# Performance work log

Hardware: AMD Instinct MI355X
Metric: run time of the kernel (lower is better)

## Reference

```python
import jax, jax.numpy as jnp
from jax import lax
import numpy as np

B, L, C = 16, 4096, 512
G = 8            # n_groups
CG = C // G      # group_dim = 64
WD = 4           # weather_dim
ORF = 10.0       # offset_range_factor


def conv1d(x, w, b=None):
    # x: [N, Cin, L], w: [Cout, Cin, 3], stride 1, padding 1
    y = lax.conv_general_dilated(x, w, window_strides=(1,), padding=[(1, 1)],
                                 dimension_numbers=('NCH', 'OIH', 'NCH'))
    if b is not None:
        y = y + b[None, :, None]
    return y


def group_norm(x, gamma, beta, groups=4, eps=1e-5):
    N, Cc, Ln = x.shape
    xr = x.reshape(N, groups, Cc // groups, Ln)
    mu = xr.mean(axis=(2, 3), keepdims=True)
    var = ((xr - mu) ** 2).mean(axis=(2, 3), keepdims=True)
    xn = ((xr - mu) / jnp.sqrt(var + eps)).reshape(N, Cc, Ln)
    return xn * gamma[None, :, None] + beta[None, :, None]


def grid_sample_bilinear_border(inp, grid):
    # Faithful torch F.grid_sample(mode='bilinear', padding_mode='border', align_corners=True)
    # inp: [N, C, H, W]; grid: [N, Ho, Wo, 2], grid[...,0]=x (width coord), grid[...,1]=y (height coord)
    N, Cc, H, W = inp.shape
    _, Ho, Wo, _ = grid.shape
    gx, gy = grid[..., 0], grid[..., 1]
    ix = jnp.clip((gx + 1.0) * 0.5 * (W - 1), 0.0, W - 1)  # border padding clamps coords
    iy = jnp.clip((gy + 1.0) * 0.5 * (H - 1), 0.0, H - 1)
    ix0f = jnp.floor(ix); iy0f = jnp.floor(iy)
    wx = ix - ix0f; wy = iy - iy0f
    ix0 = jnp.clip(ix0f.astype(jnp.int32), 0, W - 1)
    iy0 = jnp.clip(iy0f.astype(jnp.int32), 0, H - 1)
    ix1 = jnp.clip(ix0 + 1, 0, W - 1)
    iy1 = jnp.clip(iy0 + 1, 0, H - 1)
    flat = inp.reshape(N, Cc, H * W)
    def gather(iyk, ixk):
        idx = (iyk * W + ixk).reshape(N, 1, Ho * Wo)
        return jnp.take_along_axis(flat, idx, axis=2).reshape(N, Cc, Ho, Wo)
    v00 = gather(iy0, ix0); v01 = gather(iy0, ix1)
    v10 = gather(iy1, ix0); v11 = gather(iy1, ix1)
    wx = wx[:, None, :, :]; wy = wy[:, None, :, :]
    return (v00 * (1 - wy) * (1 - wx) + v01 * (1 - wy) * wx
            + v10 * wy * (1 - wx) + v11 * wy * wx)


def _forward(x, x_ext, w1, b1, gn_g, gn_b, w2, b2, w3, gate):
    xt = jnp.transpose(x, (0, 2, 1))              # [B, C, L]
    xg = xt.reshape(B * G, CG, L)                 # [B*G, CG, L]
    xe = jnp.transpose(x_ext, (0, 2, 1))          # [B, WD, L]
    xe = jnp.tile(xe, (G, 1, 1))                  # torch .repeat(n_groups,1,1)
    pin = jnp.concatenate([xg, xe], axis=1)       # [B*G, CG+WD, L]
    h = jax.nn.gelu(group_norm(conv1d(pin, w1, b1), gn_g, gn_b), approximate=False)
    h = jax.nn.gelu(conv1d(h, w2, b2), approximate=False)
    offset = jnp.tanh(conv1d(h, w3)) * ORF        # [B*G, 1, L]
    off_n = offset * (2.0 / (L - 1.0))
    ref = (jnp.linspace(0.5, L - 0.5, L, dtype=x.dtype) / (L - 1.0)) * 2.0 - 1.0
    grid_x = jnp.clip(ref[None, None, :, None] + off_n[..., None], -1.0, 1.0)  # [B*G,1,L,1]
    grid = jnp.concatenate([grid_x, jnp.zeros_like(grid_x)], axis=-1)
    grid = jnp.transpose(grid, (0, 2, 1, 3))      # [B*G, L, 1, 2]
    xs = grid_sample_bilinear_border(xg[..., None], grid)[..., 0]  # [B*G, CG, L]
    x_out = xg + jnp.tanh(gate) * xs
    x_out = x_out.reshape(B, C, L)
    return jnp.transpose(x_out, (0, 2, 1)), offset


def setup_inputs() -> dict:
    key = jax.random.key(0)
    ks = jax.random.split(key, 8)
    s = 0.05
    return {
        'x': jax.random.normal(ks[0], (B, L, C), jnp.float32),
        'x_ext': jax.random.normal(ks[1], (B, L, WD), jnp.float32),
        'w1': jax.random.normal(ks[2], (64, CG + WD, 3), jnp.float32) * s,
        'b1': jax.random.normal(ks[3], (64,), jnp.float32) * s,
        'gn_g': jnp.ones((64,), jnp.float32),
        'gn_b': jnp.zeros((64,), jnp.float32),
        'w2': jax.random.normal(ks[4], (32, 64, 3), jnp.float32) * s,
        'b2': jax.random.normal(ks[5], (32,), jnp.float32) * s,
        'w3': jax.random.normal(ks[6], (1, 32, 3), jnp.float32) * s,
        'gate': jnp.array([0.5], jnp.float32),
    }


def reference(x, x_ext, w1, b1, gn_g, gn_b, w2, b2, w3, gate):
    return _forward(x, x_ext, w1, b1, gn_g, gn_b, w2, b2, w3, gate)
```

## Files before the change

### kernel.cpp

```cpp
#include <hip/hip_runtime.h>
#include <hip/hip_bf16.h>

#define BB 16
#define LL 4096
#define CC 512
#define NG 128
#define IC1 68
#define OC1 64
#define OC2 32

typedef short short8 __attribute__((ext_vector_type(8)));
typedef float f32x4 __attribute__((ext_vector_type(4)));

__device__ inline ushort f2b(float f) {
    __hip_bfloat16 h = __float2bfloat16(f);
    return *reinterpret_cast<ushort*>(&h);
}
__device__ inline float b2f(ushort u) {
    __hip_bfloat16 h;
    *reinterpret_cast<ushort*>(&h) = u;
    return __bfloat162float(h);
}
__device__ inline float fast_tanh(float y) {
    float e = __expf(2.0f * y);
    return 1.0f - 2.0f / (e + 1.0f);
}
__device__ inline float fast_gelu(float x) {
    float y = x * (0.7978845608f + 0.0356774081f * x * x);
    return 0.5f * x * (1.0f + fast_tanh(y));
}

__global__ __launch_bounds__(256) void k_prep(const float* __restrict__ x,
    const float* __restrict__ w1, const float* __restrict__ w2,
    const float* __restrict__ gate,
    ushort* __restrict__ w1b, ushort* __restrict__ w2b, float* __restrict__ corr)
{
    int idx = blockIdx.x * 256 + threadIdx.x;
    if (idx < 18432) {
        int k = idx / 6144; int r = idx - k * 6144;
        int oc = r / 96;    int icp = r - oc * 96;
        float v = (icp < IC1) ? w1[(oc * IC1 + icp) * 3 + k] : 0.0f;
        w1b[idx] = f2b(v);
    } else if (idx < 24576) {
        int j = idx - 18432;
        int k = j / 2048; int r = j - k * 2048;
        int oc = r / 64;  int ic = r - oc * 64;
        w2b[j] = f2b(w2[(oc * OC1 + ic) * 3 + k]);
    } else if (idx < 32768) {
        int i3 = idx - 24576;
        int b = i3 >> 9; int ch = i3 & 511;
        float tg = tanhf(gate[0]);
        corr[i3] = tg * 0.5f *
            (x[((size_t)(b * LL + 2047)) * CC + ch] +
             x[((size_t)(b * LL + 2048)) * CC + ch]);
    }
}

#define KA_ROWS 130
#define KA_STR  104
template<bool FULL>
__device__ __forceinline__ void ka_body(ushort* pin,
    const float* __restrict__ x, const float* __restrict__ xe,
    const float* __restrict__ b1, const ushort* __restrict__ w1b,
    const float* __restrict__ corr, float* __restrict__ part,
    float* __restrict__ out, ushort* __restrict__ xbf, int n, int lt)
{
    const int b = n >> 3, g = n & 7, be = n & 15;
    const int l0 = lt * 128;
    const int t = threadIdx.x;
    const int q = t & 15;

    {
        const float4 corrv = *(const float4*)&corr[(b << 9) + g * 64 + q * 4];
        const float* xb = &x[((size_t)b * LL + (l0 - 1)) * CC + g * 64 + q * 4];
        float* ob = &out[((size_t)b * LL + (l0 - 1)) * CC + g * 64 + q * 4];
        ushort* xbb = &xbf[((size_t)n * LL + (l0 - 1)) * 64 + q * 4];
#pragma unroll
        for (int i = 0; i < 9; ++i) {
            int pos = t + i * 256;
            if (pos < KA_ROWS * 16) {
                int li = pos >> 4;
                float4 v;
                if (FULL) {
                    v = *(const float4*)(xb + (size_t)li * CC);
                } else {
                    int l = l0 - 1 + li;
                    v = make_float4(0.f, 0.f, 0.f, 0.f);
                    if (l >= 0 && l < LL) v = *(const float4*)(xb + (size_t)li * CC);
                }
                uint lo = (uint)f2b(v.x) | ((uint)f2b(v.y) << 16);
                uint hi = (uint)f2b(v.z) | ((uint)f2b(v.w) << 16);
                uint2 pk = make_uint2(lo, hi);
                if (li >= 1 && li <= 128) {
                    float4 o;
                    o.x = v.x + corrv.x; o.y = v.y + corrv.y;
                    o.z = v.z + corrv.z; o.w = v.w + corrv.w;
                    *(float4*)(ob + (size_t)li * CC) = o;
                    *(uint2*)(xbb + (size_t)li * 64) = pk;
                }
                *(uint2*)&pin[li * KA_STR + q * 4] = pk;
            }
        }
    }
    if (t < KA_ROWS) {
        int l = l0 - 1 + t;
        float4 v = make_float4(0.f, 0.f, 0.f, 0.f);
        if (FULL || (l >= 0 && l < LL))
            v = *(const float4*)&xe[(size_t)(be * LL + l) * 4];
        uint lo = (uint)f2b(v.x) | ((uint)f2b(v.y) << 16);
        uint hi = (uint)f2b(v.z) | ((uint)f2b(v.w) << 16);
        *(uint2*)&pin[t * KA_STR + 64] = make_uint2(lo, hi);
    }
#pragma unroll
    for (int i = 0; i < 4; ++i) {
        int pos = t + i * 256;
        if (pos < KA_ROWS * 7) {
            int li = pos / 7, j = pos - li * 7;
            *(uint2*)&pin[li * KA_STR + 68 + j * 4] = make_uint2(0u, 0u);
        }
    }
    __syncthreads();

    const int lane = t & 63;
    const int w = t >> 6;
    const int och = w & 1, lh = w >> 1;
    const int m = lane & 15, h = lane >> 4;

    short8 fa[2][9];
#pragma unroll
    for (int mi = 0; mi < 2; ++mi)
#pragma unroll
        for (int k = 0; k < 3; ++k)
#pragma unroll
            for (int c = 0; c < 3; ++c)
                fa[mi][k * 3 + c] = *(const short8*)&w1b[
                    (size_t)(k * 64 + och * 32 + mi * 16 + m) * 96 + c * 32 + h * 8];

    f32x4 acc[2][4] = {};
#pragma unroll
    for (int tt = 0; tt < 4; ++tt) {
        const int rowbase = lh * 64 + tt * 16 + m;
#pragma unroll
        for (int k = 0; k < 3; ++k) {
#pragma unroll
            for (int c = 0; c < 3; ++c) {
                short8 fb = *(const short8*)&pin[(rowbase + k) * KA_STR + c * 32 + h * 8];
                acc[0][tt] = __builtin_amdgcn_mfma_f32_16x16x32_bf16(fa[0][k * 3 + c], fb, acc[0][tt], 0, 0, 0);
                acc[1][tt] = __builtin_amdgcn_mfma_f32_16x16x32_bf16(fa[1][k * 3 + c], fb, acc[1][tt], 0, 0, 0);
            }
        }
    }

#pragma unroll
    for (int mi = 0; mi < 2; ++mi) {
        float bias[4];
#pragma unroll
        for (int r = 0; r < 4; ++r)
            bias[r] = b1[och * 32 + mi * 16 + h * 4 + r];
        float s1 = 0.f, s2 = 0.f;
#pragma unroll
        for (int tt = 0; tt < 4; ++tt) {
            float v0 = acc[mi][tt][0] + bias[0];
            float v1 = acc[mi][tt][1] + bias[1];
            float v2 = acc[mi][tt][2] + bias[2];
            float v3 = acc[mi][tt][3] + bias[3];
            s1 += v0 + v1 + v2 + v3;
            s2 += v0 * v0 + v1 * v1 + v2 * v2 + v3 * v3;
        }
#pragma unroll
        for (int off = 32; off > 0; off >>= 1) {
            s1 += __shfl_down(s1, off, 64);
            s2 += __shfl_down(s2, off, 64);
        }
        if (lane == 0) {
            int gidx = och * 2 + mi;
            part[(((size_t)n * 4 + gidx) * 64 + lt * 2 + lh) * 2 + 0] = s1;
            part[(((size_t)n * 4 + gidx) * 64 + lt * 2 + lh) * 2 + 1] = s2;
        }
    }
}

__global__ __launch_bounds__(256) void ka_stats(const float* __restrict__ x,
    const float* __restrict__ xe, const float* __restrict__ b1,
    const ushort* __restrict__ w1b, const float* __restrict__ corr,
    float* __restrict__ part, float* __restrict__ out, ushort* __restrict__ xbf)
{
    __shared__ ushort pin[KA_ROWS * KA_STR];
    const int n = blockIdx.y, lt = blockIdx.x;
    if (lt >= 1 && lt <= 30)
        ka_body<true>(pin, x, xe, b1, w1b, corr, part, out, xbf, n, lt);
    else
        ka_body<false>(pin, x, xe, b1, w1b, corr, part, out, xbf, n, lt);
}

#define BT 60
#define XR 66
#define P2S  72
#define H2S  66
template<bool FULL>
__device__ __forceinline__ void kb_body(ushort* smem, float* sstats,
    const float* __restrict__ xe, const ushort* __restrict__ xbf,
    const float* __restrict__ part, const float* __restrict__ b1,
    const ushort* __restrict__ w1b, const float* __restrict__ gn_g,
    const float* __restrict__ gn_b, const float* __restrict__ b2,
    const ushort* __restrict__ w2b, const float* __restrict__ w3,
    float* __restrict__ offs, int n, int lt)
{
    ushort* pin = smem;
    ushort* xeb = smem + 4224;
    ushort* p2  = smem;
    ushort* h2b = smem + 4752;
    const int be = n & 15;
    const int l0 = lt * BT;
    const int t = threadIdx.x;
    const int lane = t & 63;
    const int w = t >> 6;

#pragma unroll
    for (int gg = 0; gg < 2; ++gg) {
        int gidx = w * 2 + gg;
        float2 p = *(const float2*)&part[(((size_t)n * 4 + gidx) * 64 + lane) * 2];
        float s1 = p.x, s2 = p.y;
#pragma unroll
        for (int off = 32; off > 0; off >>= 1) {
            s1 += __shfl_down(s1, off, 64);
            s2 += __shfl_down(s2, off, 64);
        }
        if (lane == 0) {
            float mean = s1 * (1.0f / 65536.0f);
            float var  = s2 * (1.0f / 65536.0f) - mean * mean;
            sstats[gidx * 2 + 0] = mean;
            sstats[gidx * 2 + 1] = 1.0f / sqrtf(var + 1e-5f);
        }
    }

    {
        const uint4* xs = (const uint4*)(xbf + ((size_t)n * LL + (l0 - 3)) * 64);
#pragma unroll
        for (int i = 0; i < 5; ++i) {
            int s = t + i * 128;
            if (s < XR * 8) {
                int row = s >> 3, ch = s & 7;
                uint4 v;
                if (FULL) {
                    v = xs[s];
                } else {
                    int l = l0 - 3 + row;
                    v = make_uint4(0u, 0u, 0u, 0u);
                    if (l >= 0 && l < LL) v = xs[s];
                }
                ((uint4*)pin)[(row << 3) | (ch ^ (row & 7))] = v;
            }
        }
    }
    if (t < XR) {
        int l = l0 - 3 + t;
        float4 v = make_float4(0.f, 0.f, 0.f, 0.f);
        if (FULL || (l >= 0 && l < LL))
            v = *(const float4*)&xe[(size_t)(be * LL + l) * 4];
        uint lo = (uint)f2b(v.x) | ((uint)f2b(v.y) << 16);
        uint hi = (uint)f2b(v.z) | ((uint)f2b(v.w) << 16);
        int sw = t & 3;
        uint4 z = make_uint4(0u, 0u, 0u, 0u);
        ((uint4*)xeb)[(t << 2) | (0 ^ sw)] = make_uint4(lo, hi, 0u, 0u);
        ((uint4*)xeb)[(t << 2) | (1 ^ sw)] = z;
        ((uint4*)xeb)[(t << 2) | (2 ^ sw)] = z;
        ((uint4*)xeb)[(t << 2) | (3 ^ sw)] = z;
    }
    __syncthreads();

    const int m = lane & 15, h = lane >> 4;

    short8 fa[2][9];
#pragma unroll
    for (int mi = 0; mi < 2; ++mi)
#pragma unroll
        for (int k = 0; k < 3; ++k)
#pragma unroll
            for (int c = 0; c < 3; ++c)
                fa[mi][k * 3 + c] = *(const short8*)&w1b[
                    (size_t)(k * 64 + w * 32 + mi * 16 + m) * 96 + c * 32 + h * 8];

    f32x4 acc[2][4] = {};
#pragma unroll
    for (int tt = 0; tt < 4; ++tt) {
        const int p = tt * 16 + m;
#pragma unroll
        for (int k = 0; k < 3; ++k) {
            const int row = p + k;
#pragma unroll
            for (int c = 0; c < 3; ++c) {
                short8 fb;
                if (c < 2)
                    fb = *(const short8*)&pin[(size_t)(((row << 3) | ((c * 4 + h) ^ (row & 7))) << 3)];
                else
                    fb = *(const short8*)&xeb[(size_t)(((row << 2) | (h ^ (row & 3))) << 3)];
                acc[0][tt] = __builtin_amdgcn_mfma_f32_16x16x32_bf16(fa[0][k * 3 + c], fb, acc[0][tt], 0, 0, 0);
                acc[1][tt] = __builtin_amdgcn_mfma_f32_16x16x32_bf16(fa[1][k * 3 + c], fb, acc[1][tt], 0, 0, 0);
            }
        }
    }
    __syncthreads();

#pragma unroll
    for (int mi = 0; mi < 2; ++mi) {
        int gi = w * 2 + mi;
        float mean = sstats[gi * 2], istd = sstats[gi * 2 + 1];
        float A_[4], B_[4];
#pragma unroll
        for (int r = 0; r < 4; ++r) {
            int oc = w * 32 + mi * 16 + h * 4 + r;
            float ga = gn_g[oc];
            A_[r] = istd * ga;
            B_[r] = gn_b[oc] + (b1[oc] - mean) * A_[r];
        }
#pragma unroll
        for (int tt = 0; tt < 4; ++tt) {
            int p = tt * 16 + m;
            uint2 pk = make_uint2(0u, 0u);
            int l = l0 - 2 + p;
            if (FULL || (l >= 0 && l < LL)) {
                float v0 = fast_gelu(fmaf(acc[mi][tt][0], A_[0], B_[0]));
                float v1 = fast_gelu(fmaf(acc[mi][tt][1], A_[1], B_[1]));
                float v2 = fast_gelu(fmaf(acc[mi][tt][2], A_[2], B_[2]));
                float v3 = fast_gelu(fmaf(acc[mi][tt][3], A_[3], B_[3]));
                pk.x = (uint)f2b(v0) | ((uint)f2b(v1) << 16);
                pk.y = (uint)f2b(v2) | ((uint)f2b(v3) << 16);
            }
            *(uint2*)&p2[p * P2S + w * 32 + mi * 16 + h * 4] = pk;
        }
    }
    __syncthreads();

    short8 fa2[6];
#pragma unroll
    for (int k = 0; k < 3; ++k)
#pragma unroll
        for (int c = 0; c < 2; ++c)
            fa2[k * 2 + c] = *(const short8*)&w2b[
                (size_t)(k * 32 + w * 16 + m) * 64 + c * 32 + h * 8];

    float bias2[4];
#pragma unroll
    for (int r = 0; r < 4; ++r)
        bias2[r] = b2[w * 16 + h * 4 + r];

    f32x4 acc2[4] = {};
#pragma unroll
    for (int u = 0; u < 4; ++u) {
        const int jb = u * 16 + m;
#pragma unroll
        for (int k = 0; k < 3; ++k) {
#pragma unroll
            for (int c = 0; c < 2; ++c) {
                short8 fb = *(const short8*)&p2[(jb + k) * P2S + c * 32 + h * 8];
                acc2[u] = __builtin_amdgcn_mfma_f32_16x16x32_bf16(fa2[k * 2 + c], fb, acc2[u], 0, 0, 0);
            }
        }
    }
#pragma unroll
    for (int u = 0; u < 4; ++u) {
        int j = u * 16 + m;
        int lj = l0 - 1 + j;
#pragma unroll
        for (int r = 0; r < 4; ++r) {
            int oc = w * 16 + h * 4 + r;
            float v = 0.f;
            if (FULL || (lj >= 0 && lj < LL))
                v = fast_gelu(acc2[u][r] + bias2[r]);
            h2b[oc * H2S + j] = f2b(v);
        }
    }
    __syncthreads();

    if (t < 2 * BT) {
        int qq = t >> 1, half = t & 1;
        int ic0 = half * 16;
        float a = 0.f;
#pragma unroll
        for (int ic = 0; ic < 16; ++ic) {
            int icc = ic0 + ic;
            float v0 = b2f(h2b[icc * H2S + qq]);
            float v1 = b2f(h2b[icc * H2S + qq + 1]);
            float v2 = b2f(h2b[icc * H2S + qq + 2]);
            a = fmaf(w3[icc * 3 + 0], v0, a);
            a = fmaf(w3[icc * 3 + 1], v1, a);
            a = fmaf(w3[icc * 3 + 2], v2, a);
        }
        a += __shfl_xor(a, 1, 64);
        if (half == 0) {
            int l = l0 + qq;
            if (FULL || l < LL)
                offs[(size_t)n * LL + l] = fast_tanh(a) * 10.0f;
        }
    }
}

__global__ __launch_bounds__(128, 4) void kb_fused(const float* __restrict__ xe,
    const ushort* __restrict__ xbf, const float* __restrict__ part,
    const float* __restrict__ b1, const ushort* __restrict__ w1b,
    const float* __restrict__ gn_g, const float* __restrict__ gn_b,
    const float* __restrict__ b2, const ushort* __restrict__ w2b,
    const float* __restrict__ w3, float* __restrict__ offs)
{
    __shared__ ushort smem[6864];
    __shared__ float sstats[8];
    const int n = blockIdx.y, lt = blockIdx.x;
    if (lt >= 1 && lt <= 67)
        kb_body<true >(smem, sstats, xe, xbf, part, b1, w1b, gn_g, gn_b, b2, w2b, w3, offs, n, lt);
    else
        kb_body<false>(smem, sstats, xe, xbf, part, b1, w1b, gn_g, gn_b, b2, w2b, w3, offs, n, lt);
}

extern "C" void kernel_launch(void* const* d_in, const int* in_sizes, int n_in,
                              void* d_out, int out_size, void* d_ws, size_t ws_size,
                              hipStream_t stream)
{
    const float* x    = (const float*)d_in[0];
    const float* xext = (const float*)d_in[1];
    const float* w1   = (const float*)d_in[2];
    const float* b1   = (const float*)d_in[3];
    const float* gng  = (const float*)d_in[4];
    const float* gnb  = (const float*)d_in[5];
    const float* w2   = (const float*)d_in[6];
    const float* b2   = (const float*)d_in[7];
    const float* w3   = (const float*)d_in[8];
    const float* gate = (const float*)d_in[9];

    float* out  = (float*)d_out;
    float* offs = out + (size_t)BB * LL * CC;

    char* ws = (char*)d_ws;
    float* part = (float*)(ws);
    ushort* w1b = (ushort*)(ws + 262144);
    ushort* w2b = (ushort*)(ws + 299008);
    float* corr = (float*)(ws + 311296);
    ushort* xbf = (ushort*)(ws + 344064);

    k_prep<<<128, 256, 0, stream>>>(x, w1, w2, gate, w1b, w2b, corr);
    dim3 g1(32, NG);
    ka_stats<<<g1, 256, 0, stream>>>(x, xext, b1, w1b, corr, part, out, xbf);
    dim3 g3(69, NG);
    kb_fused<<<g3, 128, 0, stream>>>(xext, xbf, part, b1, w1b, gng, gnb, b2, w2b,
                                     w3, offs);
}
```

Baseline: 166.8 us.

## Restructure conv1 stats kernel to per-wave register tiles without shared memory

The first conv kernel no longer stages a 130-row bf16 tile in LDS behind a block barrier. Each wave now handles 16 sequence positions, loads the three shifted input rows straight from global into MFMA B-fragments and reads weight fragments from global (cache). Per-wave partial GroupNorm sums go to a larger partial buffer that the second kernel reduces in four steps. This removes LDS traffic and the barrier, but it reads each input row three times from global/cache and reloads weights per k and per tile.

```diff
diff --git a/kernel.cpp b/kernel.cpp
--- a/kernel.cpp
+++ b/kernel.cpp
@@ -28,6 +28,18 @@
 __device__ inline float fast_gelu(float x) {
     float y = x * (0.7978845608f + 0.0356774081f * x * x);
     return 0.5f * x * (1.0f + fast_tanh(y));
+}
+__device__ inline short8 pack8(float4 a, float4 b) {
+    short8 r;
+    uint* u = (uint*)&r;
+    u[0] = (uint)f2b(a.x) | ((uint)f2b(a.y) << 16);
+    u[1] = (uint)f2b(a.z) | ((uint)f2b(a.w) << 16);
+    u[2] = (uint)f2b(b.x) | ((uint)f2b(b.y) << 16);
+    u[3] = (uint)f2b(b.z) | ((uint)f2b(b.w) << 16);
+    return r;
+}
+__device__ inline float4 add4(float4 a, float4 b) {
+    return make_float4(a.x + b.x, a.y + b.y, a.z + b.z, a.w + b.w);
 }
 
 __global__ __launch_bounds__(256) void k_prep(const float* __restrict__ x,
@@ -56,141 +68,102 @@
     }
 }
 
-#define KA_ROWS 130
-#define KA_STR  104
 template<bool FULL>
-__device__ __forceinline__ void ka_body(ushort* pin,
+__device__ __forceinline__ void ka_wave(
     const float* __restrict__ x, const float* __restrict__ xe,
     const float* __restrict__ b1, const ushort* __restrict__ w1b,
     const float* __restrict__ corr, float* __restrict__ part,
-    float* __restrict__ out, ushort* __restrict__ xbf, int n, int lt)
-{
+    float* __restrict__ out, ushort* __restrict__ xbf, int n, int l0)
+{
+    const int lane = threadIdx.x & 63;
+    const int m = lane & 15, h = lane >> 4;
     const int b = n >> 3, g = n & 7, be = n & 15;
-    const int l0 = lt * 128;
-    const int t = threadIdx.x;
-    const int q = t & 15;
+
+    f32x4 acc[4] = {};
+    float4 k1lo[2], k1hi[2];
+    short8 k1f[2];
+
+#pragma unroll
+    for (int k = 0; k < 3; ++k) {
+        const int row = l0 + m + k - 1;
+        const bool ok = FULL || ((unsigned)row < (unsigned)LL);
+        const float* xp = x + ((size_t)b * LL + row) * CC + g * 64 + h * 8;
+#pragma unroll
+        for (int c = 0; c < 2; ++c) {
+            float4 lo = make_float4(0.f, 0.f, 0.f, 0.f);
+            float4 hi = make_float4(0.f, 0.f, 0.f, 0.f);
+            if (ok) {
+                lo = *(const float4*)(xp + c * 32);
+                hi = *(const float4*)(xp + c * 32 + 4);
+            }
+            short8 fb = pack8(lo, hi);
+            if (k == 1) { k1lo[c] = lo; k1hi[c] = hi; k1f[c] = fb; }
+#pragma unroll
+            for (int mt = 0; mt < 4; ++mt) {
+                short8 fa = *(const short8*)&w1b[
+                    (size_t)(k * 64 + mt * 16 + m) * 96 + c * 32 + h * 8];
+                acc[mt] = __builtin_amdgcn_mfma_f32_16x16x32_bf16(fa, fb, acc[mt], 0, 0, 0);
+            }
+        }
+        float4 xv = make_float4(0.f, 0.f, 0.f, 0.f);
+        if (h == 0 && ok) xv = *(const float4*)(xe + ((size_t)be * LL + row) * 4);
+        short8 fb2 = pack8(xv, make_float4(0.f, 0.f, 0.f, 0.f));
+#pragma unroll
+        for (int mt = 0; mt < 4; ++mt) {
+            short8 fa = *(const short8*)&w1b[
+                (size_t)(k * 64 + mt * 16 + m) * 96 + 64 + h * 8];
+            acc[mt] = __builtin_amdgcn_mfma_f32_16x16x32_bf16(fa, fb2, acc[mt], 0, 0, 0);
+        }
+    }
 
     {
-        const float4 corrv = *(const float4*)&corr[(b << 9) + g * 64 + q * 4];
-        const float* xb = &x[((size_t)b * LL + (l0 - 1)) * CC + g * 64 + q * 4];
-        float* ob = &out[((size_t)b * LL + (l0 - 1)) * CC + g * 64 + q * 4];
-        ushort* xbb = &xbf[((size_t)n * LL + (l0 - 1)) * 64 + q * 4];
-#pragma unroll
-        for (int i = 0; i < 9; ++i) {
-            int pos = t + i * 256;
-            if (pos < KA_ROWS * 16) {
-                int li = pos >> 4;
-                float4 v;
-                if (FULL) {
-                    v = *(const float4*)(xb + (size_t)li * CC);
-                } else {
-                    int l = l0 - 1 + li;
-                    v = make_float4(0.f, 0.f, 0.f, 0.f);
-                    if (l >= 0 && l < LL) v = *(const float4*)(xb + (size_t)li * CC);
-                }
-                uint lo = (uint)f2b(v.x) | ((uint)f2b(v.y) << 16);
-                uint hi = (uint)f2b(v.z) | ((uint)f2b(v.w) << 16);
-                uint2 pk = make_uint2(lo, hi);
-                if (li >= 1 && li <= 128) {
-                    float4 o;
-                    o.x = v.x + corrv.x; o.y = v.y + corrv.y;
-                    o.z = v.z + corrv.z; o.w = v.w + corrv.w;
-                    *(float4*)(ob + (size_t)li * CC) = o;
-                    *(uint2*)(xbb + (size_t)li * 64) = pk;
-                }
-                *(uint2*)&pin[li * KA_STR + q * 4] = pk;
-            }
-        }
-    }
-    if (t < KA_ROWS) {
-        int l = l0 - 1 + t;
-        float4 v = make_float4(0.f, 0.f, 0.f, 0.f);
-        if (FULL || (l >= 0 && l < LL))
-            v = *(const float4*)&xe[(size_t)(be * LL + l) * 4];
-        uint lo = (uint)f2b(v.x) | ((uint)f2b(v.y) << 16);
-        uint hi = (uint)f2b(v.z) | ((uint)f2b(v.w) << 16);
-        *(uint2*)&pin[t * KA_STR + 64] = make_uint2(lo, hi);
-    }
-#pragma unroll
-    for (int i = 0; i < 4; ++i) {
-        int pos = t + i * 256;
-        if (pos < KA_ROWS * 7) {
-            int li = pos / 7, j = pos - li * 7;
-            *(uint2*)&pin[li * KA_STR + 68 + j * 4] = make_uint2(0u, 0u);
-        }
-    }
-    __syncthreads();
-
-    const int lane = t & 63;
-    const int w = t >> 6;
-    const int och = w & 1, lh = w >> 1;
-    const int m = lane & 15, h = lane >> 4;
-
-    short8 fa[2][9];
-#pragma unroll
-    for (int mi = 0; mi < 2; ++mi)
-#pragma unroll
-        for (int k = 0; k < 3; ++k)
-#pragma unroll
-            for (int c = 0; c < 3; ++c)
-                fa[mi][k * 3 + c] = *(const short8*)&w1b[
-                    (size_t)(k * 64 + och * 32 + mi * 16 + m) * 96 + c * 32 + h * 8];
-
-    f32x4 acc[2][4] = {};
-#pragma unroll
-    for (int tt = 0; tt < 4; ++tt) {
-        const int rowbase = lh * 64 + tt * 16 + m;
-#pragma unroll
-        for (int k = 0; k < 3; ++k) {
-#pragma unroll
-            for (int c = 0; c < 3; ++c) {
-                short8 fb = *(const short8*)&pin[(rowbase + k) * KA_STR + c * 32 + h * 8];
-                acc[0][tt] = __builtin_amdgcn_mfma_f32_16x16x32_bf16(fa[0][k * 3 + c], fb, acc[0][tt], 0, 0, 0);
-                acc[1][tt] = __builtin_amdgcn_mfma_f32_16x16x32_bf16(fa[1][k * 3 + c], fb, acc[1][tt], 0, 0, 0);
-            }
-        }
-    }
-
-#pragma unroll
-    for (int mi = 0; mi < 2; ++mi) {
-        float bias[4];
-#pragma unroll
-        for (int r = 0; r < 4; ++r)
-            bias[r] = b1[och * 32 + mi * 16 + h * 4 + r];
-        float s1 = 0.f, s2 = 0.f;
-#pragma unroll
-        for (int tt = 0; tt < 4; ++tt) {
-            float v0 = acc[mi][tt][0] + bias[0];
-            float v1 = acc[mi][tt][1] + bias[1];
-            float v2 = acc[mi][tt][2] + bias[2];
-            float v3 = acc[mi][tt][3] + bias[3];
-            s1 += v0 + v1 + v2 + v3;
-            s2 += v0 * v0 + v1 * v1 + v2 * v2 + v3 * v3;
-        }
+        const int l = l0 + m;
+        const int cb = (b << 9) + g * 64 + h * 8;
+        float4 ca0 = *(const float4*)&corr[cb];
+        float4 ca1 = *(const float4*)&corr[cb + 4];
+        float4 cb0 = *(const float4*)&corr[cb + 32];
+        float4 cb1 = *(const float4*)&corr[cb + 36];
+        float* op = out + ((size_t)b * LL + l) * CC + g * 64 + h * 8;
+        *(float4*)(op)      = add4(k1lo[0], ca0);
+        *(float4*)(op + 4)  = add4(k1hi[0], ca1);
+        *(float4*)(op + 32) = add4(k1lo[1], cb0);
+        *(float4*)(op + 36) = add4(k1hi[1], cb1);
+        ushort* bp = xbf + ((size_t)n * LL + l) * 64 + h * 8;
+        *(short8*)(bp)      = k1f[0];
+        *(short8*)(bp + 32) = k1f[1];
+    }
+
+    const int seg = l0 >> 4;
+#pragma unroll
+    for (int mt = 0; mt < 4; ++mt) {
+        float4 bv = *(const float4*)&b1[mt * 16 + h * 4];
+        float v0 = acc[mt][0] + bv.x, v1 = acc[mt][1] + bv.y;
+        float v2 = acc[mt][2] + bv.z, v3 = acc[mt][3] + bv.w;
+        float a = (v0 + v1) + (v2 + v3);
+        float q = v0 * v0 + v1 * v1 + v2 * v2 + v3 * v3;
 #pragma unroll
         for (int off = 32; off > 0; off >>= 1) {
-            s1 += __shfl_down(s1, off, 64);
-            s2 += __shfl_down(s2, off, 64);
+            a += __shfl_xor(a, off, 64);
+            q += __shfl_xor(q, off, 64);
         }
         if (lane == 0) {
-            int gidx = och * 2 + mi;
-            part[(((size_t)n * 4 + gidx) * 64 + lt * 2 + lh) * 2 + 0] = s1;
-            part[(((size_t)n * 4 + gidx) * 64 + lt * 2 + lh) * 2 + 1] = s2;
-        }
-    }
-}
-
-__global__ __launch_bounds__(256) void ka_stats(const float* __restrict__ x,
+            float* pp = part + (((size_t)n * 4 + mt) * 256 + seg) * 2;
+            pp[0] = a; pp[1] = q;
+        }
+    }
+}
+
+__global__ __launch_bounds__(256, 4) void ka_conv(const float* __restrict__ x,
     const float* __restrict__ xe, const float* __restrict__ b1,
     const ushort* __restrict__ w1b, const float* __restrict__ corr,
     float* __restrict__ part, float* __restrict__ out, ushort* __restrict__ xbf)
 {
-    __shared__ ushort pin[KA_ROWS * KA_STR];
-    const int n = blockIdx.y, lt = blockIdx.x;
-    if (lt >= 1 && lt <= 30)
-        ka_body<true>(pin, x, xe, b1, w1b, corr, part, out, xbf, n, lt);
+    const int n = blockIdx.y, blk = blockIdx.x;
+    const int l0 = (blk * 4 + (threadIdx.x >> 6)) * 16;
+    if (blk >= 1 && blk <= 62)
+        ka_wave<true >(x, xe, b1, w1b, corr, part, out, xbf, n, l0);
     else
-        ka_body<false>(pin, x, xe, b1, w1b, corr, part, out, xbf, n, lt);
+        ka_wave<false>(x, xe, b1, w1b, corr, part, out, xbf, n, l0);
 }
 
 #define BT 60
@@ -219,8 +192,13 @@
 #pragma unroll
     for (int gg = 0; gg < 2; ++gg) {
         int gidx = w * 2 + gg;
-        float2 p = *(const float2*)&part[(((size_t)n * 4 + gidx) * 64 + lane) * 2];
-        float s1 = p.x, s2 = p.y;
+        const float2* pp = (const float2*)&part[(((size_t)n * 4 + gidx) * 256) * 2];
+        float s1 = 0.f, s2 = 0.f;
+#pragma unroll
+        for (int j = 0; j < 4; ++j) {
+            float2 p = pp[lane + j * 64];
+            s1 += p.x; s2 += p.y;
+        }
 #pragma unroll
         for (int off = 32; off > 0; off >>= 1) {
             s1 += __shfl_down(s1, off, 64);
@@ -432,14 +410,14 @@
 
     char* ws = (char*)d_ws;
     float* part = (float*)(ws);
-    ushort* w1b = (ushort*)(ws + 262144);
-    ushort* w2b = (ushort*)(ws + 299008);
-    float* corr = (float*)(ws + 311296);
-    ushort* xbf = (ushort*)(ws + 344064);
+    ushort* w1b = (ushort*)(ws + 1048576);
+    ushort* w2b = (ushort*)(ws + 1085440);
+    float* corr = (float*)(ws + 1097728);
+    ushort* xbf = (ushort*)(ws + 1130496);
 
     k_prep<<<128, 256, 0, stream>>>(x, w1, w2, gate, w1b, w2b, corr);
-    dim3 g1(32, NG);
-    ka_stats<<<g1, 256, 0, stream>>>(x, xext, b1, w1b, corr, part, out, xbf);
+    dim3 g1(64, NG);
+    ka_conv<<<g1, 256, 0, stream>>>(x, xext, b1, w1b, corr, part, out, xbf);
     dim3 g3(69, NG);
     kb_fused<<<g3, 128, 0, stream>>>(xext, xbf, part, b1, w1b, gng, gnb, b2, w2b,
                                      w3, offs);
```

After: 253.5 us. 1.52x slower.

## Make conv1 stats kernel persistent over four tiles with register prefetch

Applied to the files above, without the earlier changes.

The first conv/stats kernel now runs each block over four consecutive 128-row tiles, prefetching the next tile's x and x_ext into registers while the current tile is staged to shared memory and run through MFMA. The grid shrinks from 32 to 8 blocks per group. Each wave now owns 16 output channels across all 128 rows, which changes the partial-stats layout to 32 entries per group, so the consumer kernel reads 32 lanes. This aims to hide global-load latency behind MFMA work, but fewer blocks and more registers per thread (launch bounds 256,3) may reduce occupancy and parallelism.

```diff
diff --git a/kernel.cpp b/kernel.cpp
--- a/kernel.cpp
+++ b/kernel.cpp
@@ -58,59 +58,124 @@
 
 #define KA_ROWS 130
 #define KA_STR  104
-template<bool FULL>
-__device__ __forceinline__ void ka_body(ushort* pin,
+
+struct KaRegs { float4 xq[9]; float4 xev; };
+
+__device__ __forceinline__ void ka_load(KaRegs& r,
     const float* __restrict__ x, const float* __restrict__ xe,
-    const float* __restrict__ b1, const ushort* __restrict__ w1b,
-    const float* __restrict__ corr, float* __restrict__ part,
-    float* __restrict__ out, ushort* __restrict__ xbf, int n, int lt)
-{
-    const int b = n >> 3, g = n & 7, be = n & 15;
-    const int l0 = lt * 128;
-    const int t = threadIdx.x;
+    int b, int be, int g, int l0, int t)
+{
     const int q = t & 15;
-
-    {
-        const float4 corrv = *(const float4*)&corr[(b << 9) + g * 64 + q * 4];
-        const float* xb = &x[((size_t)b * LL + (l0 - 1)) * CC + g * 64 + q * 4];
-        float* ob = &out[((size_t)b * LL + (l0 - 1)) * CC + g * 64 + q * 4];
-        ushort* xbb = &xbf[((size_t)n * LL + (l0 - 1)) * 64 + q * 4];
-#pragma unroll
-        for (int i = 0; i < 9; ++i) {
-            int pos = t + i * 256;
-            if (pos < KA_ROWS * 16) {
-                int li = pos >> 4;
-                float4 v;
-                if (FULL) {
-                    v = *(const float4*)(xb + (size_t)li * CC);
-                } else {
-                    int l = l0 - 1 + li;
-                    v = make_float4(0.f, 0.f, 0.f, 0.f);
-                    if (l >= 0 && l < LL) v = *(const float4*)(xb + (size_t)li * CC);
-                }
-                uint lo = (uint)f2b(v.x) | ((uint)f2b(v.y) << 16);
-                uint hi = (uint)f2b(v.z) | ((uint)f2b(v.w) << 16);
-                uint2 pk = make_uint2(lo, hi);
-                if (li >= 1 && li <= 128) {
-                    float4 o;
-                    o.x = v.x + corrv.x; o.y = v.y + corrv.y;
-                    o.z = v.z + corrv.z; o.w = v.w + corrv.w;
-                    *(float4*)(ob + (size_t)li * CC) = o;
-                    *(uint2*)(xbb + (size_t)li * 64) = pk;
-                }
-                *(uint2*)&pin[li * KA_STR + q * 4] = pk;
-            }
+    const float* xb = x + ((size_t)b * LL + (l0 - 1)) * CC + g * 64 + q * 4;
+#pragma unroll
+    for (int i = 0; i < 9; ++i) {
+        int pos = t + i * 256;
+        if (pos < KA_ROWS * 16) {
+            int li = pos >> 4;
+            int l = l0 - 1 + li;
+            r.xq[i] = make_float4(0.f, 0.f, 0.f, 0.f);
+            if ((unsigned)l < (unsigned)LL)
+                r.xq[i] = *(const float4*)(xb + (size_t)li * CC);
         }
     }
     if (t < KA_ROWS) {
         int l = l0 - 1 + t;
-        float4 v = make_float4(0.f, 0.f, 0.f, 0.f);
-        if (FULL || (l >= 0 && l < LL))
-            v = *(const float4*)&xe[(size_t)(be * LL + l) * 4];
-        uint lo = (uint)f2b(v.x) | ((uint)f2b(v.y) << 16);
-        uint hi = (uint)f2b(v.z) | ((uint)f2b(v.w) << 16);
+        r.xev = make_float4(0.f, 0.f, 0.f, 0.f);
+        if ((unsigned)l < (unsigned)LL)
+            r.xev = *(const float4*)(xe + ((size_t)be * LL + l) * 4);
+    }
+}
+
+__device__ __forceinline__ void ka_write(ushort* pin, const KaRegs& r,
+    const float4 corr0, float* __restrict__ out, ushort* __restrict__ xbf,
+    int b, int g, int n, int l0, int t)
+{
+    const int q = t & 15;
+#pragma unroll
+    for (int i = 0; i < 9; ++i) {
+        int pos = t + i * 256;
+        if (pos < KA_ROWS * 16) {
+            int li = pos >> 4;
+            uint lo = (uint)f2b(r.xq[i].x) | ((uint)f2b(r.xq[i].y) << 16);
+            uint hi = (uint)f2b(r.xq[i].z) | ((uint)f2b(r.xq[i].w) << 16);
+            uint2 pk = make_uint2(lo, hi);
+            *(uint2*)&pin[li * KA_STR + q * 4] = pk;
+            if (li >= 1 && li <= 128) {
+                int l = l0 - 1 + li;
+                float4 o;
+                o.x = r.xq[i].x + corr0.x; o.y = r.xq[i].y + corr0.y;
+                o.z = r.xq[i].z + corr0.z; o.w = r.xq[i].w + corr0.w;
+                *(float4*)(out + ((size_t)b * LL + l) * CC + g * 64 + q * 4) = o;
+                *(uint2*)(xbf + ((size_t)n * LL + l) * 64 + q * 4) = pk;
+            }
+        }
+    }
+    if (t < KA_ROWS) {
+        uint lo = (uint)f2b(r.xev.x) | ((uint)f2b(r.xev.y) << 16);
+        uint hi = (uint)f2b(r.xev.z) | ((uint)f2b(r.xev.w) << 16);
         *(uint2*)&pin[t * KA_STR + 64] = make_uint2(lo, hi);
     }
+}
+
+__device__ __forceinline__ void ka_mfma(const ushort* pin,
+    const float* __restrict__ b1, const ushort* __restrict__ w1b,
+    float* __restrict__ part, int n, int lt, int w, int lane)
+{
+    const int m = lane & 15, h = lane >> 4;
+    short8 fa[9];
+#pragma unroll
+    for (int k = 0; k < 3; ++k)
+#pragma unroll
+        for (int c = 0; c < 3; ++c)
+            fa[k * 3 + c] = *(const short8*)&w1b[
+                (size_t)(k * 64 + w * 16 + m) * 96 + c * 32 + h * 8];
+
+    float4 bv = *(const float4*)&b1[w * 16 + h * 4];
+    float s1 = 0.f, s2 = 0.f;
+#pragma unroll
+    for (int tt = 0; tt < 8; ++tt) {
+        f32x4 acc = {};
+        const int rowbase = tt * 16 + m;
+#pragma unroll
+        for (int k = 0; k < 3; ++k)
+#pragma unroll
+            for (int c = 0; c < 3; ++c) {
+                short8 fb = *(const short8*)&pin[(rowbase + k) * KA_STR + c * 32 + h * 8];
+                acc = __builtin_amdgcn_mfma_f32_16x16x32_bf16(fa[k * 3 + c], fb, acc, 0, 0, 0);
+            }
+        float v0 = acc[0] + bv.x, v1 = acc[1] + bv.y;
+        float v2 = acc[2] + bv.z, v3 = acc[3] + bv.w;
+        s1 += (v0 + v1) + (v2 + v3);
+        s2 += v0 * v0 + v1 * v1 + v2 * v2 + v3 * v3;
+    }
+#pragma unroll
+    for (int off = 32; off > 0; off >>= 1) {
+        s1 += __shfl_xor(s1, off, 64);
+        s2 += __shfl_xor(s2, off, 64);
+    }
+    if (lane == 0) {
+        float* pp = part + (((size_t)n * 4 + w) * 32 + lt) * 2;
+        pp[0] = s1; pp[1] = s2;
+    }
+}
+
+__global__ __launch_bounds__(256, 3) void ka_conv(const float* __restrict__ x,
+    const float* __restrict__ xe, const float* __restrict__ b1,
+    const ushort* __restrict__ w1b, const float* __restrict__ corr,
+    float* __restrict__ part, float* __restrict__ out, ushort* __restrict__ xbf)
+{
+    __shared__ ushort pin[KA_ROWS * KA_STR];
+    const int n = blockIdx.y, chunk = blockIdx.x;
+    const int b = n >> 3, g = n & 7, be = n & 15;
+    const int t = threadIdx.x;
+    const int lane = t & 63, w = t >> 6;
+    const int q = t & 15;
+
+    const float4 corr0 = *(const float4*)&corr[(b << 9) + g * 64 + q * 4];
+
+    KaRegs rg[2];
+    ka_load(rg[0], x, xe, b, be, g, chunk * 4 * 128, t);
+
 #pragma unroll
     for (int i = 0; i < 4; ++i) {
         int pos = t + i * 256;
@@ -119,78 +184,18 @@
             *(uint2*)&pin[li * KA_STR + 68 + j * 4] = make_uint2(0u, 0u);
         }
     }
-    __syncthreads();
-
-    const int lane = t & 63;
-    const int w = t >> 6;
-    const int och = w & 1, lh = w >> 1;
-    const int m = lane & 15, h = lane >> 4;
-
-    short8 fa[2][9];
-#pragma unroll
-    for (int mi = 0; mi < 2; ++mi)
-#pragma unroll
-        for (int k = 0; k < 3; ++k)
-#pragma unroll
-            for (int c = 0; c < 3; ++c)
-                fa[mi][k * 3 + c] = *(const short8*)&w1b[
-                    (size_t)(k * 64 + och * 32 + mi * 16 + m) * 96 + c * 32 + h * 8];
-
-    f32x4 acc[2][4] = {};
-#pragma unroll
-    for (int tt = 0; tt < 4; ++tt) {
-        const int rowbase = lh * 64 + tt * 16 + m;
-#pragma unroll
-        for (int k = 0; k < 3; ++k) {
-#pragma unroll
-            for (int c = 0; c < 3; ++c) {
-                short8 fb = *(const short8*)&pin[(rowbase + k) * KA_STR + c * 32 + h * 8];
-                acc[0][tt] = __builtin_amdgcn_mfma_f32_16x16x32_bf16(fa[0][k * 3 + c], fb, acc[0][tt], 0, 0, 0);
-                acc[1][tt] = __builtin_amdgcn_mfma_f32_16x16x32_bf16(fa[1][k * 3 + c], fb, acc[1][tt], 0, 0, 0);
-            }
-        }
-    }
-
-#pragma unroll
-    for (int mi = 0; mi < 2; ++mi) {
-        float bias[4];
-#pragma unroll
-        for (int r = 0; r < 4; ++r)
-            bias[r] = b1[och * 32 + mi * 16 + h * 4 + r];
-        float s1 = 0.f, s2 = 0.f;
-#pragma unroll
-        for (int tt = 0; tt < 4; ++tt) {
-            float v0 = acc[mi][tt][0] + bias[0];
-            float v1 = acc[mi][tt][1] + bias[1];
-            float v2 = acc[mi][tt][2] + bias[2];
-            float v3 = acc[mi][tt][3] + bias[3];
-            s1 += v0 + v1 + v2 + v3;
-            s2 += v0 * v0 + v1 * v1 + v2 * v2 + v3 * v3;
-        }
-#pragma unroll
-        for (int off = 32; off > 0; off >>= 1) {
-            s1 += __shfl_down(s1, off, 64);
-            s2 += __shfl_down(s2, off, 64);
-        }
-        if (lane == 0) {
-            int gidx = och * 2 + mi;
-            part[(((size_t)n * 4 + gidx) * 64 + lt * 2 + lh) * 2 + 0] = s1;
-            part[(((size_t)n * 4 + gidx) * 64 + lt * 2 + lh) * 2 + 1] = s2;
-        }
-    }
-}
-
-__global__ __launch_bounds__(256) void ka_stats(const float* __restrict__ x,
-    const float* __restrict__ xe, const float* __restrict__ b1,
-    const ushort* __restrict__ w1b, const float* __restrict__ corr,
-    float* __restrict__ part, float* __restrict__ out, ushort* __restrict__ xbf)
-{
-    __shared__ ushort pin[KA_ROWS * KA_STR];
-    const int n = blockIdx.y, lt = blockIdx.x;
-    if (lt >= 1 && lt <= 30)
-        ka_body<true>(pin, x, xe, b1, w1b, corr, part, out, xbf, n, lt);
-    else
-        ka_body<false>(pin, x, xe, b1, w1b, corr, part, out, xbf, n, lt);
+
+#pragma unroll
+    for (int it = 0; it < 4; ++it) {
+        const int lt = chunk * 4 + it;
+        const int l0 = lt * 128;
+        __syncthreads();
+        ka_write(pin, rg[it & 1], corr0, out, xbf, b, g, n, l0, t);
+        if (it < 3)
+            ka_load(rg[(it + 1) & 1], x, xe, b, be, g, (lt + 1) * 128, t);
+        __syncthreads();
+        ka_mfma(pin, b1, w1b, part, n, lt, w, lane);
+    }
 }
 
 #define BT 60
@@ -219,12 +224,15 @@
 #pragma unroll
     for (int gg = 0; gg < 2; ++gg) {
         int gidx = w * 2 + gg;
-        float2 p = *(const float2*)&part[(((size_t)n * 4 + gidx) * 64 + lane) * 2];
-        float s1 = p.x, s2 = p.y;
+        float s1 = 0.f, s2 = 0.f;
+        if (lane < 32) {
+            float2 p = *(const float2*)&part[(((size_t)n * 4 + gidx) * 32 + lane) * 2];
+            s1 = p.x; s2 = p.y;
+        }
 #pragma unroll
         for (int off = 32; off > 0; off >>= 1) {
-            s1 += __shfl_down(s1, off, 64);
-            s2 += __shfl_down(s2, off, 64);
+            s1 += __shfl_xor(s1, off, 64);
+            s2 += __shfl_xor(s2, off, 64);
         }
         if (lane == 0) {
             float mean = s1 * (1.0f / 65536.0f);
@@ -432,14 +440,14 @@
 
     char* ws = (char*)d_ws;
     float* part = (float*)(ws);
-    ushort* w1b = (ushort*)(ws + 262144);
-    ushort* w2b = (ushort*)(ws + 299008);
-    float* corr = (float*)(ws + 311296);
-    ushort* xbf = (ushort*)(ws + 344064);
+    ushort* w1b = (ushort*)(ws + 131072);
+    ushort* w2b = (ushort*)(ws + 167936);
+    float* corr = (float*)(ws + 180224);
+    ushort* xbf = (ushort*)(ws + 212992);
 
     k_prep<<<128, 256, 0, stream>>>(x, w1, w2, gate, w1b, w2b, corr);
-    dim3 g1(32, NG);
-    ka_stats<<<g1, 256, 0, stream>>>(x, xext, b1, w1b, corr, part, out, xbf);
+    dim3 g1(8, NG);
+    ka_conv<<<g1, 256, 0, stream>>>(x, xext, b1, w1b, corr, part, out, xbf);
     dim3 g3(69, NG);
     kb_fused<<<g3, 128, 0, stream>>>(xext, xbf, part, b1, w1b, gng, gnb, b2, w2b,
                                      w3, offs);
```

Measured after the change: 221.3 us. 1.33x slower.
